# Optimization experiments

Measured on AMD Instinct MI355X. Metric: run time of the kernel, lower is better.

The kernel has to match this reference:

```python
import jax, jax.numpy as jnp
import numpy as np

NEG_INF = -1e9  # additive mask value (every row attends to itself, so softmax is safe)


def setup_inputs() -> dict:
    D, H, N = 256, 8, 4096
    key = jax.random.key(0)
    ks = jax.random.split(key, 7)
    slots = jax.random.normal(ks[0], (1, N, D), dtype=jnp.float32)
    batch_idx = jnp.sort(jax.random.randint(ks[1], (N,), 0, 16)).astype(jnp.int32)
    s_in = 1.0 / np.sqrt(D)
    w_in = jax.random.uniform(ks[2], (3 * D, D), jnp.float32, -s_in, s_in)
    b_in = jnp.zeros((3 * D,), jnp.float32)
    w_out = jax.random.uniform(ks[3], (D, D), jnp.float32, -s_in, s_in)
    b_out = jnp.zeros((D,), jnp.float32)
    ln_gamma = jnp.ones((D,), jnp.float32)
    ln_beta = jnp.zeros((D,), jnp.float32)
    return {"slots": slots, "batch_idx": batch_idx, "w_in": w_in, "b_in": b_in,
            "w_out": w_out, "b_out": b_out, "ln_gamma": ln_gamma, "ln_beta": ln_beta}


def _mha_block_diag(x, batch_idx, w_in, b_in, w_out, b_out, num_heads):
    # x: [N, D]
    N, D = x.shape
    hd = D // num_heads
    qkv = x @ w_in.T + b_in                      # [N, 3D]
    q, k, v = jnp.split(qkv, 3, axis=-1)
    q = q.reshape(N, num_heads, hd).transpose(1, 0, 2)   # [H, N, hd]
    k = k.reshape(N, num_heads, hd).transpose(1, 0, 2)
    v = v.reshape(N, num_heads, hd).transpose(1, 0, 2)
    scale = 1.0 / np.sqrt(hd)
    scores = jnp.einsum('hnd,hmd->hnm', q, k) * scale    # [H, N, N]
    mask = batch_idx[:, None] != batch_idx[None, :]      # True = blocked
    scores = jnp.where(mask[None], NEG_INF, scores)
    attn = jax.nn.softmax(scores, axis=-1)
    out = jnp.einsum('hnm,hmd->hnd', attn, v)            # [H, N, hd]
    out = out.transpose(1, 0, 2).reshape(N, D)
    return out @ w_out.T + b_out


def _layer_norm(x, gamma, beta, eps=1e-5):
    mu = jnp.mean(x, axis=-1, keepdims=True)
    var = jnp.mean(jnp.square(x - mu), axis=-1, keepdims=True)
    return (x - mu) * jax.lax.rsqrt(var + eps) * gamma + beta


def reference(slots, batch_idx, w_in, b_in, w_out, b_out, ln_gamma, ln_beta):
    # slots: [1, N, D]; dropout prob is 0.0 (eval-mode reference)
    x = slots[0]
    delta = _mha_block_diag(x, batch_idx, w_in, b_in, w_out, b_out, num_heads=8)
    out = _layer_norm(x + delta, ln_gamma, ln_beta)
    return out[None]
```

## Files before the change

### kernel.cpp

```cpp
#include <hip/hip_runtime.h>
#include <hip/hip_bf16.h>

#define NROWS 4096
#define DMODEL 256
#define NHEADS 8
#define HD 32

typedef __attribute__((ext_vector_type(8))) short short8;
typedef __attribute__((ext_vector_type(4))) float f32x4;

__global__ __launch_bounds__(256) void prep_kernel(
    const float* __restrict__ slots, const float* __restrict__ w_in,
    const float* __restrict__ w_out, const int* __restrict__ bidx,
    __hip_bfloat16* __restrict__ Abf, __hip_bfloat16* __restrict__ Winb,
    __hip_bfloat16* __restrict__ Woutb, int* __restrict__ segs) {
  const int bid = blockIdx.x;
  const float* src;
  __hip_bfloat16* dst;
  int i;
  if (bid < 1024)      { src = slots; dst = Abf;   i = (bid * 256 + (int)threadIdx.x) * 4; }
  else if (bid < 1216) { src = w_in;  dst = Winb;  i = ((bid - 1024) * 256 + (int)threadIdx.x) * 4; }
  else if (bid < 1280) { src = w_out; dst = Woutb; i = ((bid - 1216) * 256 + (int)threadIdx.x) * 4; }
  else {
    const int r = (bid - 1280) * 256 + threadIdx.x;
    const int b = bidx[r];
    if (r == 0 || bidx[r - 1] != b) segs[b] = r;
    if (r == NROWS - 1 || bidx[r + 1] != b) segs[16 + b] = r + 1;
    return;
  }
  const float4 v = *(const float4*)(src + i);
  __hip_bfloat162 lo, hi;
  lo.x = __float2bfloat16(v.x); lo.y = __float2bfloat16(v.y);
  hi.x = __float2bfloat16(v.z); hi.y = __float2bfloat16(v.w);
  *(__hip_bfloat162*)(dst + i) = lo;
  *(__hip_bfloat162*)(dst + i + 2) = hi;
}

__device__ __forceinline__ void load_lds16(const void* g, void* l) {
  __builtin_amdgcn_global_load_lds(
      (const __attribute__((address_space(1))) unsigned int*)g,
      (__attribute__((address_space(3))) unsigned int*)l, 16, 0, 0);
}

template<bool SCATTER>
__global__ __launch_bounds__(256) void gemm_mfma(
    const __hip_bfloat16* __restrict__ A, const __hip_bfloat16* __restrict__ B,
    const float* __restrict__ bias, float* __restrict__ C,
    __hip_bfloat16* __restrict__ Qo, __hip_bfloat16* __restrict__ Ko,
    __hip_bfloat16* __restrict__ Vo,
    int Nd, int K) {
  __shared__ __hip_bfloat16 As[128][32];
  __shared__ __hip_bfloat16 Bs[128][32];
  const int tid  = threadIdx.x;
  const int w    = tid >> 6;
  const int lane = tid & 63;
  const int lo16 = lane & 15;
  const int quad = lane >> 4;
  const int bm = blockIdx.y * 128;
  const int bn = blockIdx.x * 128;
  const int wm = (w & 1) * 64;
  const int wn = (w >> 1) * 64;

  f32x4 acc[4][4] = {};
  const int fbase = w * 2048;

  for (int k0 = 0; k0 < K; k0 += 32) {
    #pragma unroll
    for (int inst = 0; inst < 2; inst++) {
      const int f   = fbase + inst * 1024 + lane * 16;
      const int row = f >> 6;
      const int kb  = (f & 63) >> 1;
      load_lds16(A + (size_t)(bm + row) * K + k0 + kb,
                 (char*)&As[0][0] + fbase + inst * 1024);
      load_lds16(B + (size_t)(bn + row) * K + k0 + kb,
                 (char*)&Bs[0][0] + fbase + inst * 1024);
    }
    __syncthreads();
    short8 af[4], bf[4];
    #pragma unroll
    for (int i = 0; i < 4; i++) {
      af[i] = *(const short8*)&As[wm + i * 16 + lo16][quad * 8];
      bf[i] = *(const short8*)&Bs[wn + i * 16 + lo16][quad * 8];
    }
    #pragma unroll
    for (int mi = 0; mi < 4; mi++)
      #pragma unroll
      for (int ni = 0; ni < 4; ni++)
        acc[mi][ni] = __builtin_amdgcn_mfma_f32_16x16x32_bf16(
            af[mi], bf[ni], acc[mi][ni], 0, 0, 0);
    __syncthreads();
  }

  #pragma unroll
  for (int mi = 0; mi < 4; mi++) {
    const int rbase = bm + wm + mi * 16 + quad * 4;
    #pragma unroll
    for (int ni = 0; ni < 4; ni++) {
      const int col = bn + wn + ni * 16 + lo16;
      const float bv = bias[col];
      #pragma unroll
      for (int r = 0; r < 4; r++) {
        const int n = rbase + r;
        const float v = acc[mi][ni][r] + bv;
        if (SCATTER) {
          const int sel = col >> 8;
          const int h = (col & 255) >> 5;
          const int d = col & 31;
          const __hip_bfloat16 bv16 = __float2bfloat16(v);
          if (sel == 0)      Qo[((size_t)h * NROWS + n) * HD + d] = bv16;
          else if (sel == 1) Ko[((size_t)h * NROWS + n) * HD + d] = bv16;
          else               Vo[((size_t)h * HD + d) * NROWS + n] = bv16;
        } else {
          C[(size_t)n * Nd + col] = v;
        }
      }
    }
  }
}

__global__ __launch_bounds__(256, 2) void attn_mfma(
    const __hip_bfloat16* __restrict__ Qb,
    const __hip_bfloat16* __restrict__ Kb,
    const __hip_bfloat16* __restrict__ Vt,
    const int* __restrict__ bidx,
    const int* __restrict__ segs,
    __hip_bfloat16* __restrict__ out)
{
  __shared__ __align__(16) __hip_bfloat16 Plds_all[4][16][136];
  const int wv   = threadIdx.x >> 6;
  const int lane = threadIdx.x & 63;
  const int wid  = blockIdx.x * 4 + wv;
  const int qt   = wid >> 3;
  const int h    = wid & 7;
  const int r0   = qt * 16;
  const int lo16 = lane & 15;
  const int quad = lane >> 4;
  __hip_bfloat16 (*Plds)[136] = Plds_all[wv];

  int st[4], en[4];
  #pragma unroll
  for (int r = 0; r < 4; r++) {
    const int b = bidx[r0 + quad * 4 + r];
    st[r] = segs[b];
    en[r] = segs[16 + b];
  }

  const int kstart = segs[bidx[r0]] & ~31;
  const int kend   = segs[16 + bidx[r0 + 15]];

  const short8 qf = *(const short8*)(Qb + ((size_t)h * NROWS + r0 + lo16) * HD + quad * 8);

  f32x4 o0 = {0.f, 0.f, 0.f, 0.f}, o1 = {0.f, 0.f, 0.f, 0.f};
  float m[4], l[4];
  #pragma unroll
  for (int r = 0; r < 4; r++) { m[r] = -1e30f; l[r] = 0.0f; }

  const float scale = 0.17677669529663687f;

  for (int c0 = kstart; c0 < kend; c0 += 128) {
    short8 kf[8];
    #pragma unroll
    for (int j = 0; j < 8; j++) {
      const int cc = min(c0 + j * 16 + lo16, NROWS - 1);
      kf[j] = *(const short8*)(Kb + ((size_t)h * NROWS + cc) * HD + quad * 8);
    }
    short8 vf[8];
    #pragma unroll
    for (int t = 0; t < 4; t++) {
      const int vc = min(c0 + t * 32 + quad * 8, NROWS - 8);
      vf[2 * t]     = *(const short8*)(Vt + ((size_t)h * HD + lo16) * NROWS + vc);
      vf[2 * t + 1] = *(const short8*)(Vt + ((size_t)h * HD + 16 + lo16) * NROWS + vc);
    }
    f32x4 s[8];
    const f32x4 z = {0.f, 0.f, 0.f, 0.f};
    #pragma unroll
    for (int j = 0; j < 8; j++)
      s[j] = __builtin_amdgcn_mfma_f32_16x16x32_bf16(qf, kf[j], z, 0, 0, 0);

    #pragma unroll
    for (int r = 0; r < 4; r++) {
      float sc[8];
      #pragma unroll
      for (int j = 0; j < 8; j++) {
        const int col = c0 + j * 16 + lo16;
        const bool ok = (col >= st[r]) & (col < en[r]);
        sc[j] = ok ? s[j][r] * scale : -1e30f;
      }
      float mx = sc[0];
      #pragma unroll
      for (int j = 1; j < 8; j++) mx = fmaxf(mx, sc[j]);
      mx = fmaxf(mx, __shfl_xor(mx, 1));
      mx = fmaxf(mx, __shfl_xor(mx, 2));
      mx = fmaxf(mx, __shfl_xor(mx, 4));
      mx = fmaxf(mx, __shfl_xor(mx, 8));
      const float nm = fmaxf(m[r], mx);
      const float alpha = __expf(m[r] - nm);
      float ps = 0.0f;
      #pragma unroll
      for (int j = 0; j < 8; j++) {
        const float p = (sc[j] > -5e29f) ? __expf(sc[j] - nm) : 0.0f;
        ps += p;
        Plds[quad * 4 + r][lo16 + j * 16] = __float2bfloat16(p);
      }
      ps += __shfl_xor(ps, 1);
      ps += __shfl_xor(ps, 2);
      ps += __shfl_xor(ps, 4);
      ps += __shfl_xor(ps, 8);
      l[r] = l[r] * alpha + ps;
      m[r] = nm;
      o0[r] *= alpha;
      o1[r] *= alpha;
    }

    #pragma unroll
    for (int t = 0; t < 4; t++) {
      const short8 pf = *(const short8*)&Plds[lo16][t * 32 + quad * 8];
      o0 = __builtin_amdgcn_mfma_f32_16x16x32_bf16(pf, vf[2 * t],     o0, 0, 0, 0);
      o1 = __builtin_amdgcn_mfma_f32_16x16x32_bf16(pf, vf[2 * t + 1], o1, 0, 0, 0);
    }
  }

  #pragma unroll
  for (int r = 0; r < 4; r++) {
    const float inv = 1.0f / l[r];
    const int row = r0 + quad * 4 + r;
    out[(size_t)row * DMODEL + h * HD + lo16]      = __float2bfloat16(o0[r] * inv);
    out[(size_t)row * DMODEL + h * HD + 16 + lo16] = __float2bfloat16(o1[r] * inv);
  }
}

__global__ __launch_bounds__(256) void ln_kernel(
    const float* __restrict__ x, const float* __restrict__ delta,
    const float* __restrict__ gamma, const float* __restrict__ beta,
    float* __restrict__ out) {
  const int n = blockIdx.x;
  const int t = threadIdx.x;
  __shared__ float red[8];
  const float v = x[(size_t)n * DMODEL + t] + delta[(size_t)n * DMODEL + t];
  float s = v;
  #pragma unroll
  for (int off = 32; off; off >>= 1) s += __shfl_xor(s, off);
  const int w = t >> 6;
  if ((t & 63) == 0) red[w] = s;
  __syncthreads();
  const float mean = (red[0] + red[1] + red[2] + red[3]) * (1.0f / DMODEL);
  const float d0 = v - mean;
  float s2 = d0 * d0;
  #pragma unroll
  for (int off = 32; off; off >>= 1) s2 += __shfl_xor(s2, off);
  if ((t & 63) == 0) red[4 + w] = s2;
  __syncthreads();
  const float var = (red[4] + red[5] + red[6] + red[7]) * (1.0f / DMODEL);
  out[(size_t)n * DMODEL + t] = d0 * rsqrtf(var + 1e-5f) * gamma[t] + beta[t];
}

extern "C" void kernel_launch(void* const* d_in, const int* in_sizes, int n_in,
                              void* d_out, int out_size, void* d_ws, size_t ws_size,
                              hipStream_t stream) {
  const float* slots  = (const float*)d_in[0];
  const int*   bidx   = (const int*)  d_in[1];
  const float* w_in   = (const float*)d_in[2];
  const float* b_in   = (const float*)d_in[3];
  const float* w_out  = (const float*)d_in[4];
  const float* b_out  = (const float*)d_in[5];
  const float* ln_g   = (const float*)d_in[6];
  const float* ln_b   = (const float*)d_in[7];
  float* out = (float*)d_out;

  char* ws = (char*)d_ws;
  __hip_bfloat16* Abf   = (__hip_bfloat16*)(ws);
  __hip_bfloat16* Qb    = (__hip_bfloat16*)(ws + (2u  << 20));
  __hip_bfloat16* Kb    = (__hip_bfloat16*)(ws + (4u  << 20));
  __hip_bfloat16* Vt    = (__hip_bfloat16*)(ws + (6u  << 20));
  __hip_bfloat16* attnb = (__hip_bfloat16*)(ws + (8u  << 20));
  float*          proj  = (float*)         (ws + (10u << 20));
  __hip_bfloat16* Winb  = (__hip_bfloat16*)(ws + (14u << 20));
  __hip_bfloat16* Woutb = (__hip_bfloat16*)(ws + (14u << 20) + (512u << 10));
  int*            segs  = (int*)           (ws + (15u << 20));

  prep_kernel<<<1296, 256, 0, stream>>>(slots, w_in, w_out, bidx,
                                        Abf, Winb, Woutb, segs);
  {
    dim3 grid(768 / 128, NROWS / 128);
    gemm_mfma<true><<<grid, 256, 0, stream>>>(Abf, Winb, b_in, nullptr,
                                              Qb, Kb, Vt, 768, DMODEL);
  }
  attn_mfma<<<(NROWS / 16) * NHEADS / 4, 256, 0, stream>>>(Qb, Kb, Vt, bidx,
                                                           segs, attnb);
  {
    dim3 grid(DMODEL / 128, NROWS / 128);
    gemm_mfma<false><<<grid, 256, 0, stream>>>(attnb, Woutb, b_out, proj,
                                               nullptr, nullptr, nullptr,
                                               DMODEL, DMODEL);
  }
  ln_kernel<<<NROWS, 256, 0, stream>>>(slots, proj, ln_g, ln_b, out);
}
```

Baseline: 120.8 us.

## Split attention keys across waves, fuse out-proj with layernorm, shrink GEMM tiles

Attention now gives each 16-row query tile and head its own block and splits the key range across the four waves in 32-key tiles. The per-wave max, sum and output are merged through shared memory at the end. The output projection is fused with the residual add and layernorm into one kernel, which drops the fp32 projection buffer and a launch. The QKV GEMM drops the LDS tiling for smaller 64x64 tiles that read fragments straight from global memory. This raises parallelism and cuts launches, at the cost of cross-wave merge overhead, smaller MFMA batches per load, and a one-pass variance formula that is less numerically stable.

```diff
diff --git a/kernel.cpp b/kernel.cpp
--- a/kernel.cpp
+++ b/kernel.cpp
@@ -36,89 +36,49 @@
   *(__hip_bfloat162*)(dst + i + 2) = hi;
 }
 
-__device__ __forceinline__ void load_lds16(const void* g, void* l) {
-  __builtin_amdgcn_global_load_lds(
-      (const __attribute__((address_space(1))) unsigned int*)g,
-      (__attribute__((address_space(3))) unsigned int*)l, 16, 0, 0);
-}
-
-template<bool SCATTER>
-__global__ __launch_bounds__(256) void gemm_mfma(
-    const __hip_bfloat16* __restrict__ A, const __hip_bfloat16* __restrict__ B,
-    const float* __restrict__ bias, float* __restrict__ C,
-    __hip_bfloat16* __restrict__ Qo, __hip_bfloat16* __restrict__ Ko,
-    __hip_bfloat16* __restrict__ Vo,
-    int Nd, int K) {
-  __shared__ __hip_bfloat16 As[128][32];
-  __shared__ __hip_bfloat16 Bs[128][32];
-  const int tid  = threadIdx.x;
-  const int w    = tid >> 6;
-  const int lane = tid & 63;
+__global__ __launch_bounds__(256, 4) void gemm_qkv(
+    const __hip_bfloat16* __restrict__ A,
+    const __hip_bfloat16* __restrict__ B,
+    const float* __restrict__ bias,
+    __hip_bfloat16* __restrict__ Qo,
+    __hip_bfloat16* __restrict__ Ko,
+    __hip_bfloat16* __restrict__ Vo) {
+  const int wv   = threadIdx.x >> 6;
+  const int lane = threadIdx.x & 63;
   const int lo16 = lane & 15;
   const int quad = lane >> 4;
-  const int bm = blockIdx.y * 128;
-  const int bn = blockIdx.x * 128;
-  const int wm = (w & 1) * 64;
-  const int wn = (w >> 1) * 64;
-
-  f32x4 acc[4][4] = {};
-  const int fbase = w * 2048;
-
-  for (int k0 = 0; k0 < K; k0 += 32) {
-    #pragma unroll
-    for (int inst = 0; inst < 2; inst++) {
-      const int f   = fbase + inst * 1024 + lane * 16;
-      const int row = f >> 6;
-      const int kb  = (f & 63) >> 1;
-      load_lds16(A + (size_t)(bm + row) * K + k0 + kb,
-                 (char*)&As[0][0] + fbase + inst * 1024);
-      load_lds16(B + (size_t)(bn + row) * K + k0 + kb,
-                 (char*)&Bs[0][0] + fbase + inst * 1024);
-    }
-    __syncthreads();
-    short8 af[4], bf[4];
-    #pragma unroll
-    for (int i = 0; i < 4; i++) {
-      af[i] = *(const short8*)&As[wm + i * 16 + lo16][quad * 8];
-      bf[i] = *(const short8*)&Bs[wn + i * 16 + lo16][quad * 8];
-    }
-    #pragma unroll
-    for (int mi = 0; mi < 4; mi++)
-      #pragma unroll
-      for (int ni = 0; ni < 4; ni++)
-        acc[mi][ni] = __builtin_amdgcn_mfma_f32_16x16x32_bf16(
-            af[mi], bf[ni], acc[mi][ni], 0, 0, 0);
-    __syncthreads();
-  }
-
-  #pragma unroll
-  for (int mi = 0; mi < 4; mi++) {
-    const int rbase = bm + wm + mi * 16 + quad * 4;
+  const int bm = blockIdx.y * 64 + wv * 16;
+  const int bn = blockIdx.x * 64;
+
+  f32x4 acc[4] = {};
+  #pragma unroll
+  for (int k0 = 0; k0 < 256; k0 += 32) {
+    const short8 af = *(const short8*)(A + (size_t)(bm + lo16) * 256 + k0 + quad * 8);
     #pragma unroll
     for (int ni = 0; ni < 4; ni++) {
-      const int col = bn + wn + ni * 16 + lo16;
-      const float bv = bias[col];
-      #pragma unroll
-      for (int r = 0; r < 4; r++) {
-        const int n = rbase + r;
-        const float v = acc[mi][ni][r] + bv;
-        if (SCATTER) {
-          const int sel = col >> 8;
-          const int h = (col & 255) >> 5;
-          const int d = col & 31;
-          const __hip_bfloat16 bv16 = __float2bfloat16(v);
-          if (sel == 0)      Qo[((size_t)h * NROWS + n) * HD + d] = bv16;
-          else if (sel == 1) Ko[((size_t)h * NROWS + n) * HD + d] = bv16;
-          else               Vo[((size_t)h * HD + d) * NROWS + n] = bv16;
-        } else {
-          C[(size_t)n * Nd + col] = v;
-        }
-      }
-    }
-  }
-}
-
-__global__ __launch_bounds__(256, 2) void attn_mfma(
+      const short8 bf = *(const short8*)(B + (size_t)(bn + ni * 16 + lo16) * 256 + k0 + quad * 8);
+      acc[ni] = __builtin_amdgcn_mfma_f32_16x16x32_bf16(af, bf, acc[ni], 0, 0, 0);
+    }
+  }
+  #pragma unroll
+  for (int ni = 0; ni < 4; ni++) {
+    const int col = bn + ni * 16 + lo16;
+    const int sel = col >> 8;
+    const int h = (col & 255) >> 5;
+    const int d = col & 31;
+    const float bv = bias[col];
+    #pragma unroll
+    for (int r = 0; r < 4; r++) {
+      const int n = bm + quad * 4 + r;
+      const __hip_bfloat16 v = __float2bfloat16(acc[ni][r] + bv);
+      if (sel == 0)      Qo[((size_t)h * NROWS + n) * HD + d] = v;
+      else if (sel == 1) Ko[((size_t)h * NROWS + n) * HD + d] = v;
+      else               Vo[((size_t)h * HD + d) * NROWS + n] = v;
+    }
+  }
+}
+
+__global__ __launch_bounds__(256, 4) void attn_mfma(
     const __hip_bfloat16* __restrict__ Qb,
     const __hip_bfloat16* __restrict__ Kb,
     const __hip_bfloat16* __restrict__ Vt,
@@ -126,16 +86,17 @@
     const int* __restrict__ segs,
     __hip_bfloat16* __restrict__ out)
 {
-  __shared__ __align__(16) __hip_bfloat16 Plds_all[4][16][136];
+  __shared__ __align__(16) __hip_bfloat16 Plds_all[4][16][40];
+  __shared__ float mld[4][16], lld[4][16];
+  __shared__ float Old[4][16][32];
   const int wv   = threadIdx.x >> 6;
   const int lane = threadIdx.x & 63;
-  const int wid  = blockIdx.x * 4 + wv;
-  const int qt   = wid >> 3;
-  const int h    = wid & 7;
+  const int qt   = blockIdx.x >> 3;
+  const int h    = blockIdx.x & 7;
   const int r0   = qt * 16;
   const int lo16 = lane & 15;
   const int quad = lane >> 4;
-  __hip_bfloat16 (*Plds)[136] = Plds_all[wv];
+  __hip_bfloat16 (*Plds)[40] = Plds_all[wv];
 
   int st[4], en[4];
   #pragma unroll
@@ -144,9 +105,9 @@
     st[r] = segs[b];
     en[r] = segs[16 + b];
   }
-
   const int kstart = segs[bidx[r0]] & ~31;
   const int kend   = segs[16 + bidx[r0 + 15]];
+  const int ntiles = (kend - kstart + 31) >> 5;
 
   const short8 qf = *(const short8*)(Qb + ((size_t)h * NROWS + r0 + lo16) * HD + quad * 8);
 
@@ -157,51 +118,38 @@
 
   const float scale = 0.17677669529663687f;
 
-  for (int c0 = kstart; c0 < kend; c0 += 128) {
-    short8 kf[8];
-    #pragma unroll
-    for (int j = 0; j < 8; j++) {
-      const int cc = min(c0 + j * 16 + lo16, NROWS - 1);
-      kf[j] = *(const short8*)(Kb + ((size_t)h * NROWS + cc) * HD + quad * 8);
-    }
-    short8 vf[8];
-    #pragma unroll
-    for (int t = 0; t < 4; t++) {
-      const int vc = min(c0 + t * 32 + quad * 8, NROWS - 8);
-      vf[2 * t]     = *(const short8*)(Vt + ((size_t)h * HD + lo16) * NROWS + vc);
-      vf[2 * t + 1] = *(const short8*)(Vt + ((size_t)h * HD + 16 + lo16) * NROWS + vc);
-    }
-    f32x4 s[8];
+  for (int t = wv; t < ntiles; t += 4) {
+    const int c0 = kstart + t * 32;
+    const int col0 = c0 + lo16;
+    const int col1 = col0 + 16;
+    const int colc0 = min(col0, NROWS - 1);
+    const int colc1 = min(col1, NROWS - 1);
+    const short8 kf0 = *(const short8*)(Kb + ((size_t)h * NROWS + colc0) * HD + quad * 8);
+    const short8 kf1 = *(const short8*)(Kb + ((size_t)h * NROWS + colc1) * HD + quad * 8);
+    const int vc = min(c0 + quad * 8, NROWS - 8);
+    const short8 vf0 = *(const short8*)(Vt + ((size_t)h * HD + lo16) * NROWS + vc);
+    const short8 vf1 = *(const short8*)(Vt + ((size_t)h * HD + 16 + lo16) * NROWS + vc);
+
     const f32x4 z = {0.f, 0.f, 0.f, 0.f};
-    #pragma unroll
-    for (int j = 0; j < 8; j++)
-      s[j] = __builtin_amdgcn_mfma_f32_16x16x32_bf16(qf, kf[j], z, 0, 0, 0);
+    f32x4 s0 = __builtin_amdgcn_mfma_f32_16x16x32_bf16(qf, kf0, z, 0, 0, 0);
+    f32x4 s1 = __builtin_amdgcn_mfma_f32_16x16x32_bf16(qf, kf1, z, 0, 0, 0);
 
     #pragma unroll
     for (int r = 0; r < 4; r++) {
-      float sc[8];
-      #pragma unroll
-      for (int j = 0; j < 8; j++) {
-        const int col = c0 + j * 16 + lo16;
-        const bool ok = (col >= st[r]) & (col < en[r]);
-        sc[j] = ok ? s[j][r] * scale : -1e30f;
-      }
-      float mx = sc[0];
-      #pragma unroll
-      for (int j = 1; j < 8; j++) mx = fmaxf(mx, sc[j]);
+      const bool ok0 = (col0 >= st[r]) & (col0 < en[r]);
+      const bool ok1 = (col1 >= st[r]) & (col1 < en[r]);
+      const float sc0 = ok0 ? s0[r] * scale : -1e30f;
+      const float sc1 = ok1 ? s1[r] * scale : -1e30f;
+      float mx = fmaxf(sc0, sc1);
       mx = fmaxf(mx, __shfl_xor(mx, 1));
       mx = fmaxf(mx, __shfl_xor(mx, 2));
       mx = fmaxf(mx, __shfl_xor(mx, 4));
       mx = fmaxf(mx, __shfl_xor(mx, 8));
       const float nm = fmaxf(m[r], mx);
       const float alpha = __expf(m[r] - nm);
-      float ps = 0.0f;
-      #pragma unroll
-      for (int j = 0; j < 8; j++) {
-        const float p = (sc[j] > -5e29f) ? __expf(sc[j] - nm) : 0.0f;
-        ps += p;
-        Plds[quad * 4 + r][lo16 + j * 16] = __float2bfloat16(p);
-      }
+      const float p0 = ok0 ? __expf(sc0 - nm) : 0.0f;
+      const float p1 = ok1 ? __expf(sc1 - nm) : 0.0f;
+      float ps = p0 + p1;
       ps += __shfl_xor(ps, 1);
       ps += __shfl_xor(ps, 2);
       ps += __shfl_xor(ps, 4);
@@ -210,48 +158,106 @@
       m[r] = nm;
       o0[r] *= alpha;
       o1[r] *= alpha;
-    }
-
-    #pragma unroll
-    for (int t = 0; t < 4; t++) {
-      const short8 pf = *(const short8*)&Plds[lo16][t * 32 + quad * 8];
-      o0 = __builtin_amdgcn_mfma_f32_16x16x32_bf16(pf, vf[2 * t],     o0, 0, 0, 0);
-      o1 = __builtin_amdgcn_mfma_f32_16x16x32_bf16(pf, vf[2 * t + 1], o1, 0, 0, 0);
-    }
-  }
-
-  #pragma unroll
-  for (int r = 0; r < 4; r++) {
-    const float inv = 1.0f / l[r];
-    const int row = r0 + quad * 4 + r;
-    out[(size_t)row * DMODEL + h * HD + lo16]      = __float2bfloat16(o0[r] * inv);
-    out[(size_t)row * DMODEL + h * HD + 16 + lo16] = __float2bfloat16(o1[r] * inv);
-  }
-}
-
-__global__ __launch_bounds__(256) void ln_kernel(
-    const float* __restrict__ x, const float* __restrict__ delta,
+      Plds[quad * 4 + r][lo16]      = __float2bfloat16(p0);
+      Plds[quad * 4 + r][lo16 + 16] = __float2bfloat16(p1);
+    }
+    const short8 pf = *(const short8*)&Plds[lo16][quad * 8];
+    o0 = __builtin_amdgcn_mfma_f32_16x16x32_bf16(pf, vf0, o0, 0, 0, 0);
+    o1 = __builtin_amdgcn_mfma_f32_16x16x32_bf16(pf, vf1, o1, 0, 0, 0);
+  }
+
+  #pragma unroll
+  for (int r = 0; r < 4; r++) {
+    const int row = quad * 4 + r;
+    Old[wv][row][lo16]      = o0[r];
+    Old[wv][row][lo16 + 16] = o1[r];
+    if (lo16 == 0) { mld[wv][row] = m[r]; lld[wv][row] = l[r]; }
+  }
+  __syncthreads();
+
+  const int row = threadIdx.x >> 4;
+  const int c   = threadIdx.x & 15;
+  float M = fmaxf(fmaxf(mld[0][row], mld[1][row]),
+                  fmaxf(mld[2][row], mld[3][row]));
+  float L = 0.f, O0 = 0.f, O1 = 0.f;
+  #pragma unroll
+  for (int w = 0; w < 4; w++) {
+    const float e = __expf(mld[w][row] - M);
+    L  += e * lld[w][row];
+    O0 += e * Old[w][row][c];
+    O1 += e * Old[w][row][c + 16];
+  }
+  const float inv = 1.0f / L;
+  const int grow = r0 + row;
+  out[(size_t)grow * DMODEL + h * HD + c]      = __float2bfloat16(O0 * inv);
+  out[(size_t)grow * DMODEL + h * HD + 16 + c] = __float2bfloat16(O1 * inv);
+}
+
+__global__ __launch_bounds__(256, 4) void gemm_out_ln(
+    const __hip_bfloat16* __restrict__ A,
+    const __hip_bfloat16* __restrict__ B,
+    const float* __restrict__ bias,
+    const float* __restrict__ x,
     const float* __restrict__ gamma, const float* __restrict__ beta,
     float* __restrict__ out) {
-  const int n = blockIdx.x;
-  const int t = threadIdx.x;
-  __shared__ float red[8];
-  const float v = x[(size_t)n * DMODEL + t] + delta[(size_t)n * DMODEL + t];
-  float s = v;
-  #pragma unroll
-  for (int off = 32; off; off >>= 1) s += __shfl_xor(s, off);
-  const int w = t >> 6;
-  if ((t & 63) == 0) red[w] = s;
+  __shared__ float red1[16][4], red2[16][4];
+  const int wv   = threadIdx.x >> 6;
+  const int lane = threadIdx.x & 63;
+  const int lo16 = lane & 15;
+  const int quad = lane >> 4;
+  const int r0 = blockIdx.x * 16;
+  const int wn = wv * 64;
+
+  f32x4 acc[4] = {};
+  #pragma unroll
+  for (int k0 = 0; k0 < 256; k0 += 32) {
+    const short8 af = *(const short8*)(A + (size_t)(r0 + lo16) * 256 + k0 + quad * 8);
+    #pragma unroll
+    for (int ni = 0; ni < 4; ni++) {
+      const short8 bf = *(const short8*)(B + (size_t)(wn + ni * 16 + lo16) * 256 + k0 + quad * 8);
+      acc[ni] = __builtin_amdgcn_mfma_f32_16x16x32_bf16(af, bf, acc[ni], 0, 0, 0);
+    }
+  }
+
+  float val[4][4];
+  float s1[4] = {}, s2[4] = {};
+  #pragma unroll
+  for (int ni = 0; ni < 4; ni++) {
+    const int col = wn + ni * 16 + lo16;
+    const float bv = bias[col];
+    #pragma unroll
+    for (int r = 0; r < 4; r++) {
+      const int row = r0 + quad * 4 + r;
+      const float v = acc[ni][r] + bv + x[(size_t)row * DMODEL + col];
+      val[ni][r] = v;
+      s1[r] += v;
+      s2[r] += v * v;
+    }
+  }
+  #pragma unroll
+  for (int r = 0; r < 4; r++) {
+    #pragma unroll
+    for (int off = 1; off < 16; off <<= 1) {
+      s1[r] += __shfl_xor(s1[r], off);
+      s2[r] += __shfl_xor(s2[r], off);
+    }
+    if (lo16 == 0) { red1[quad * 4 + r][wv] = s1[r]; red2[quad * 4 + r][wv] = s2[r]; }
+  }
   __syncthreads();
-  const float mean = (red[0] + red[1] + red[2] + red[3]) * (1.0f / DMODEL);
-  const float d0 = v - mean;
-  float s2 = d0 * d0;
-  #pragma unroll
-  for (int off = 32; off; off >>= 1) s2 += __shfl_xor(s2, off);
-  if ((t & 63) == 0) red[4 + w] = s2;
-  __syncthreads();
-  const float var = (red[4] + red[5] + red[6] + red[7]) * (1.0f / DMODEL);
-  out[(size_t)n * DMODEL + t] = d0 * rsqrtf(var + 1e-5f) * gamma[t] + beta[t];
+  #pragma unroll
+  for (int r = 0; r < 4; r++) {
+    const int lrow = quad * 4 + r;
+    const float mean = (red1[lrow][0] + red1[lrow][1] + red1[lrow][2] + red1[lrow][3]) * (1.0f / DMODEL);
+    const float ex2  = (red2[lrow][0] + red2[lrow][1] + red2[lrow][2] + red2[lrow][3]) * (1.0f / DMODEL);
+    const float rstd = rsqrtf(fmaxf(ex2 - mean * mean, 0.0f) + 1e-5f);
+    const int row = r0 + lrow;
+    #pragma unroll
+    for (int ni = 0; ni < 4; ni++) {
+      const int col = wn + ni * 16 + lo16;
+      out[(size_t)row * DMODEL + col] =
+          (val[ni][r] - mean) * rstd * gamma[col] + beta[col];
+    }
+  }
 }
 
 extern "C" void kernel_launch(void* const* d_in, const int* in_sizes, int n_in,
@@ -273,25 +279,18 @@
   __hip_bfloat16* Kb    = (__hip_bfloat16*)(ws + (4u  << 20));
   __hip_bfloat16* Vt    = (__hip_bfloat16*)(ws + (6u  << 20));
   __hip_bfloat16* attnb = (__hip_bfloat16*)(ws + (8u  << 20));
-  float*          proj  = (float*)         (ws + (10u << 20));
-  __hip_bfloat16* Winb  = (__hip_bfloat16*)(ws + (14u << 20));
-  __hip_bfloat16* Woutb = (__hip_bfloat16*)(ws + (14u << 20) + (512u << 10));
-  int*            segs  = (int*)           (ws + (15u << 20));
+  __hip_bfloat16* Winb  = (__hip_bfloat16*)(ws + (10u << 20));
+  __hip_bfloat16* Woutb = (__hip_bfloat16*)(ws + (10u << 20) + (512u << 10));
+  int*            segs  = (int*)           (ws + (11u << 20));
 
   prep_kernel<<<1296, 256, 0, stream>>>(slots, w_in, w_out, bidx,
                                         Abf, Winb, Woutb, segs);
   {
-    dim3 grid(768 / 128, NROWS / 128);
-    gemm_mfma<true><<<grid, 256, 0, stream>>>(Abf, Winb, b_in, nullptr,
-                                              Qb, Kb, Vt, 768, DMODEL);
-  }
-  attn_mfma<<<(NROWS / 16) * NHEADS / 4, 256, 0, stream>>>(Qb, Kb, Vt, bidx,
-                                                           segs, attnb);
-  {
-    dim3 grid(DMODEL / 128, NROWS / 128);
-    gemm_mfma<false><<<grid, 256, 0, stream>>>(attnb, Woutb, b_out, proj,
-                                               nullptr, nullptr, nullptr,
-                                               DMODEL, DMODEL);
-  }
-  ln_kernel<<<NROWS, 256, 0, stream>>>(slots, proj, ln_g, ln_b, out);
-}
+    dim3 grid(768 / 64, NROWS / 64);
+    gemm_qkv<<<grid, 256, 0, stream>>>(Abf, Winb, b_in, Qb, Kb, Vt);
+  }
+  attn_mfma<<<(NROWS / 16) * NHEADS, 256, 0, stream>>>(Qb, Kb, Vt, bidx,
+                                                       segs, attnb);
+  gemm_out_ln<<<NROWS / 16, 256, 0, stream>>>(attnb, Woutb, b_out, slots,
+                                              ln_g, ln_b, out);
+}
```

Result: faster. 114.9 us (-4.9%).
